# Performance work log

Measured on AMD Instinct MI355X. Metric: run time of the kernel, lower is better.

Reference implementation:

```python
import jax, jax.numpy as jnp
import numpy as np

CH = 16

_SOBEL_X = jnp.array([[-1.0, 0.0, 1.0], [-2.0, 0.0, 2.0], [-1.0, 0.0, 1.0]], dtype=jnp.float32) / 8.0
_SOBEL_Y = _SOBEL_X.T


def _depthwise3x3(x, k2d):
    # x: (B, C, H, W); k2d: (3, 3). Depthwise cross-correlation, padding=1 (matches torch.conv2d).
    c = x.shape[1]
    w = jnp.broadcast_to(k2d[None, None], (c, 1, 3, 3))
    return jax.lax.conv_general_dilated(
        x, w, window_strides=(1, 1), padding=((1, 1), (1, 1)),
        dimension_numbers=("NCHW", "OIHW", "NCHW"), feature_group_count=c)


def setup_inputs() -> dict:
    key = jax.random.key(0)
    k0, k1, k2, k3, k4 = jax.random.split(key, 5)
    B, C, H, W = 16, CH, 256, 256
    grid = jax.random.normal(k0, (B, C, H, W), dtype=jnp.float32)
    # 1x1 convs are per-pixel matmuls; store as matrices. Kaiming-ish scale.
    W1 = jax.random.normal(k1, (8 * CH, 3 * CH), dtype=jnp.float32) * (1.0 / np.sqrt(3 * CH))
    b1 = jax.random.normal(k2, (8 * CH,), dtype=jnp.float32) * 0.01
    W2 = jax.random.normal(k3, (CH, 8 * CH), dtype=jnp.float32) * (1.0 / np.sqrt(8 * CH))
    b2 = jax.random.normal(k4, (CH,), dtype=jnp.float32) * 0.01
    return {"grid": grid, "W1": W1, "b1": b1, "W2": W2, "b2": b2}


def reference(grid, W1, b1, W2, b2):
    # perception: concat(grid, sobel_x(grid), sobel_y(grid)) along channels -> (B, 3C, H, W)
    px = _depthwise3x3(grid, _SOBEL_X)
    py = _depthwise3x3(grid, _SOBEL_Y)
    perception = jnp.concatenate([grid, px, py], axis=1)
    # two-layer 1x1-conv MLP with ReLU
    h = jnp.einsum("bchw,oc->bohw", perception, W1) + b1[None, :, None, None]
    h = jax.nn.relu(h)
    out = jnp.einsum("bchw,oc->bohw", h, W2) + b2[None, :, None, None]
    return out
```

## Files before the change

### kernel.cpp

```cpp
#include <hip/hip_runtime.h>

typedef float           f32x16  __attribute__((ext_vector_type(16)));
typedef float           f32x4   __attribute__((ext_vector_type(4)));
typedef __bf16          bf16x8  __attribute__((ext_vector_type(8)));
typedef unsigned short  ushort8 __attribute__((ext_vector_type(8)));
typedef unsigned int    uint4v  __attribute__((ext_vector_type(4)));

#define MFMA(a,b,c) __builtin_amdgcn_mfma_f32_32x32x16_bf16(a, b, c, 0, 0, 0)

__device__ __forceinline__ unsigned fbits(float x) { return __builtin_bit_cast(unsigned, x); }
__device__ __forceinline__ float bitsf(unsigned u) { return __builtin_bit_cast(float, u); }

__device__ __forceinline__ void bsplit(float x, unsigned short& hi, unsigned short& lo) {
    unsigned u = fbits(x);
    hi = (unsigned short)(u >> 16);
    float rem = x - bitsf(u & 0xFFFF0000u);
    lo = (unsigned short)(fbits(rem) >> 16);
}

__global__ __launch_bounds__(256, 4) void nca_mfma3_kernel(
    const float* __restrict__ grid,
    const float* __restrict__ W1, const float* __restrict__ b1,
    const float* __restrict__ W2, const float* __restrict__ b2,
    float* __restrict__ out)
{
    __shared__ unsigned short sLDS[16640];
    float* sB1f = (float*)&sLDS[16384];

    const int tid  = threadIdx.x;
    const int l    = tid & 63;
    const int w    = tid >> 6;
    const int half = l >> 5;
    const int ol   = l & 31;

    #pragma unroll
    for (int i = 0; i < 3; ++i) {
        int sidx = tid + 256*i;
        int ls   = sidx & 63;
        int fp   = sidx >> 6;
        int kk   = fp % 3;
        int o    = (fp/3)*32 + (ls & 31);
        int k0   = kk*16 + (ls>>5)*8;
        float sc = (kk == 0) ? 1.0f : 0.125f;
        ushort8 hi8, lo8;
        #pragma unroll
        for (int j = 0; j < 8; ++j) {
            float v = W1[o*48 + k0 + j] * sc;
            unsigned short h, lo_;
            bsplit(v, h, lo_);
            hi8[j] = h; lo8[j] = lo_;
        }
        *(ushort8*)&sLDS[(fp*2 + 0)*512 + ls*8] = hi8;
        *(ushort8*)&sLDS[(fp*2 + 1)*512 + ls*8] = lo8;
    }

    {
        int kk2  = tid >> 5;
        int cidx = tid & 31;
        int o    = cidx & 15;
        int hs   = cidx >> 4;
        int k0   = kk2*16 + hs*8;
        ushort8 hi8, lo8;
        #pragma unroll
        for (int j = 0; j < 8; ++j) {
            float v = W2[o*128 + k0 + j];
            unsigned short h, lo_;
            bsplit(v, h, lo_);
            hi8[j] = h; lo8[j] = lo_;
        }
        *(ushort8*)&sLDS[12288 + (kk2*2 + 0)*256 + cidx*8] = hi8;
        *(ushort8*)&sLDS[12288 + (kk2*2 + 1)*256 + cidx*8] = lo8;
    }

    if (tid < 128) sB1f[tid] = b1[tid];

    const bool  v16 = (ol < 16);
    const float b2v = v16 ? b2[ol] : 0.0f;

    __syncthreads();

    const int w1a = l*16;
    const int w2a = 24576 + ((ol & 15) + (half << 4))*16;
    const int b1a = 4*half;

    const auto ld8 = [&](int byteoff) -> ushort8 {
        return *(const ushort8*)((const char*)sLDS + byteoff);
    };

    const int bid  = blockIdx.x;
    const int wgid = ((bid & 7) << 8) | (bid >> 3);

    const int gw = wgid*4 + w;
    const int t0 = gw*4;
    const int y  = (t0 >> 3) & 255;
    const int b  =  t0 >> 11;
    const int dyt = (y > 0)   ? -256 : 0;
    const int dyb = (y < 255) ?  256 : 0;
    const float fmt = (y > 0)   ? 1.f : 0.f;
    const float fmb = (y < 255) ? 1.f : 0.f;

    for (int i = 0; i < 4; ++i) {
        const int t  = t0 + i;
        const int x0 = (t & 7) << 5;
        const int x  = x0 + ol;

        const int   dxl = (x > 0)   ? -1 : 0;
        const int   dxr = (x < 255) ?  1 : 0;
        const float fml = (x > 0)   ? 1.f : 0.f;
        const float fmr = (x < 255) ? 1.f : 0.f;
        const float ftl = fml*fmt, ftr = fmr*fmt, fbl = fml*fmb, fbr = fmr*fmb;

        int w1ai = w1a, w2ai = w2a, b1ai = b1a;
        asm volatile("" : "+v"(w1ai), "+v"(w2ai), "+v"(b1ai));

        const int pbase = (b*16 + half*8)*65536 + y*256 + x;
        ushort8 ahi[3], alo[3];
        #pragma unroll
        for (int ci = 0; ci < 8; ++ci) {
            int ic = pbase + ci*65536;
            int it = ic + dyt, ib = ic + dyb;
            float v00 = grid[it + dxl]*ftl, v01 = grid[it]*fmt, v02 = grid[it + dxr]*ftr;
            float v10 = grid[ic + dxl]*fml, v11 = grid[ic],     v12 = grid[ic + dxr]*fmr;
            float v20 = grid[ib + dxl]*fbl, v21 = grid[ib]*fmb, v22 = grid[ib + dxr]*fbr;
            float sx = (v02 - v00) + 2.f*(v12 - v10) + (v22 - v20);
            float sy = (v20 - v00) + 2.f*(v21 - v01) + (v22 - v02);
            unsigned short h, lo_;
            bsplit(v11, h, lo_); ahi[0][ci] = h; alo[0][ci] = lo_;
            bsplit(sx,  h, lo_); ahi[1][ci] = h; alo[1][ci] = lo_;
            bsplit(sy,  h, lo_); ahi[2][ci] = h; alo[2][ci] = lo_;
        }

        f32x16 acc2;
        #pragma unroll
        for (int r = 0; r < 16; ++r) acc2[r] = b2v;

        #pragma unroll
        for (int og = 0; og < 4; ++og) {
            f32x16 acc1;
            #pragma unroll
            for (int T = 0; T < 4; ++T) {
                f32x4 q = *(const f32x4*)&sB1f[b1ai + og*32 + 8*T];
                acc1[4*T+0] = q[0]; acc1[4*T+1] = q[1];
                acc1[4*T+2] = q[2]; acc1[4*T+3] = q[3];
            }

            #pragma unroll
            for (int kk = 0; kk < 3; ++kk) {
                bf16x8 ph  = __builtin_bit_cast(bf16x8, ahi[kk]);
                bf16x8 pl  = __builtin_bit_cast(bf16x8, alo[kk]);
                bf16x8 w_h = __builtin_bit_cast(bf16x8, ld8(w1ai + ((og*3 + kk)*2 + 0)*1024));
                bf16x8 w_l = __builtin_bit_cast(bf16x8, ld8(w1ai + ((og*3 + kk)*2 + 1)*1024));
                acc1 = MFMA(w_h, ph, acc1);
                acc1 = MFMA(w_h, pl, acc1);
                acc1 = MFMA(w_l, ph, acc1);
            }

            unsigned Phi[8], Plo[8];
            #pragma unroll
            for (int T = 0; T < 4; ++T) {
                float h0 = fmaxf(acc1[4*T+0], 0.f), h1 = fmaxf(acc1[4*T+1], 0.f);
                float h2 = fmaxf(acc1[4*T+2], 0.f), h3 = fmaxf(acc1[4*T+3], 0.f);
                unsigned u0 = fbits(h0), u1 = fbits(h1), u2 = fbits(h2), u3 = fbits(h3);
                Phi[2*T+0] = (u0 >> 16) | (u1 & 0xFFFF0000u);
                Phi[2*T+1] = (u2 >> 16) | (u3 & 0xFFFF0000u);
                float r0 = h0 - bitsf(u0 & 0xFFFF0000u);
                float r1 = h1 - bitsf(u1 & 0xFFFF0000u);
                float r2 = h2 - bitsf(u2 & 0xFFFF0000u);
                float r3 = h3 - bitsf(u3 & 0xFFFF0000u);
                Plo[2*T+0] = (fbits(r0) >> 16) | (fbits(r1) & 0xFFFF0000u);
                Plo[2*T+1] = (fbits(r2) >> 16) | (fbits(r3) & 0xFFFF0000u);
            }

            #pragma unroll
            for (int c = 0; c < 2; ++c) {
                unsigned fa0 = Phi[(2*c)*2+0], fb0 = Phi[(2*c+1)*2+0];
                unsigned fa1 = Phi[(2*c)*2+1], fb1 = Phi[(2*c+1)*2+1];
                asm volatile("v_permlane32_swap_b32 %0, %1" : "+v"(fa0), "+v"(fb0));
                asm volatile("v_permlane32_swap_b32 %0, %1" : "+v"(fa1), "+v"(fb1));
                unsigned la0 = Plo[(2*c)*2+0], lb0 = Plo[(2*c+1)*2+0];
                unsigned la1 = Plo[(2*c)*2+1], lb1 = Plo[(2*c+1)*2+1];
                asm volatile("v_permlane32_swap_b32 %0, %1" : "+v"(la0), "+v"(lb0));
                asm volatile("v_permlane32_swap_b32 %0, %1" : "+v"(la1), "+v"(lb1));
                uint4v hv_ = { fa0, fa1, fb0, fb1 };
                uint4v lv_ = { la0, la1, lb0, lb1 };
                bf16x8 A2h = __builtin_bit_cast(bf16x8, hv_);
                bf16x8 A2l = __builtin_bit_cast(bf16x8, lv_);

                const int g = (og*2 + c)*2;
                bf16x8 w2h = __builtin_bit_cast(bf16x8, ld8(w2ai + (g + 0)*512));
                bf16x8 w2l = __builtin_bit_cast(bf16x8, ld8(w2ai + (g + 1)*512));
                acc2 = MFMA(A2h, w2h, acc2);
                acc2 = MFMA(A2h, w2l, acc2);
                acc2 = MFMA(A2l, w2h, acc2);
            }
        }

        if (v16) {
            const int ob = (b*16 + ol)*65536 + y*256 + x0 + half*4;
            #pragma unroll
            for (int c = 0; c < 4; ++c) {
                f32x4 v = { acc2[4*c+0], acc2[4*c+1], acc2[4*c+2], acc2[4*c+3] };
                *(f32x4*)&out[ob + c*8] = v;
            }
        }
    }
}

extern "C" void kernel_launch(void* const* d_in, const int* in_sizes, int n_in,
                              void* d_out, int out_size, void* d_ws, size_t ws_size,
                              hipStream_t stream) {
    const float* grid = (const float*)d_in[0];
    const float* W1   = (const float*)d_in[1];
    const float* b1   = (const float*)d_in[2];
    const float* W2   = (const float*)d_in[3];
    const float* b2   = (const float*)d_in[4];
    float* out = (float*)d_out;

    nca_mfma3_kernel<<<2048, 256, 0, stream>>>(grid, W1, b1, W2, b2, out);
}
```

Measured before the change: 191.4 us.

## Use 512-thread blocks, add branch-free interior stencil path, and pack bf16 halves with v_perm

```diff
diff --git a/kernel.cpp b/kernel.cpp
--- a/kernel.cpp
+++ b/kernel.cpp
@@ -8,17 +8,24 @@
 
 #define MFMA(a,b,c) __builtin_amdgcn_mfma_f32_32x32x16_bf16(a, b, c, 0, 0, 0)
 
-__device__ __forceinline__ unsigned fbits(float x) { return __builtin_bit_cast(unsigned, x); }
-__device__ __forceinline__ float bitsf(unsigned u) { return __builtin_bit_cast(float, u); }
-
-__device__ __forceinline__ void bsplit(float x, unsigned short& hi, unsigned short& lo) {
+static __device__ __forceinline__ unsigned fbits(float x) { return __builtin_bit_cast(unsigned, x); }
+static __device__ __forceinline__ float    bitsf(unsigned u) { return __builtin_bit_cast(float, u); }
+
+static __device__ __forceinline__ void bsplit(float x, unsigned short& hi, unsigned short& lo) {
     unsigned u = fbits(x);
     hi = (unsigned short)(u >> 16);
     float rem = x - bitsf(u & 0xFFFF0000u);
     lo = (unsigned short)(fbits(rem) >> 16);
 }
 
-__global__ __launch_bounds__(256, 4) void nca_mfma3_kernel(
+static __device__ __forceinline__ unsigned packhi(float e, float o) {
+    return __builtin_amdgcn_perm(fbits(o), fbits(e), 0x07060302u);
+}
+static __device__ __forceinline__ float remf(float x) {
+    return x - bitsf(fbits(x) & 0xFFFF0000u);
+}
+
+__global__ __launch_bounds__(512, 8) void nca_mfma4_kernel(
     const float* __restrict__ grid,
     const float* __restrict__ W1, const float* __restrict__ b1,
     const float* __restrict__ W2, const float* __restrict__ b2,
@@ -33,9 +40,7 @@
     const int half = l >> 5;
     const int ol   = l & 31;
 
-    #pragma unroll
-    for (int i = 0; i < 3; ++i) {
-        int sidx = tid + 256*i;
+    for (int sidx = tid; sidx < 768; sidx += 512) {
         int ls   = sidx & 63;
         int fp   = sidx >> 6;
         int kk   = fp % 3;
@@ -45,16 +50,15 @@
         ushort8 hi8, lo8;
         #pragma unroll
         for (int j = 0; j < 8; ++j) {
-            float v = W1[o*48 + k0 + j] * sc;
             unsigned short h, lo_;
-            bsplit(v, h, lo_);
+            bsplit(W1[o*48 + k0 + j] * sc, h, lo_);
             hi8[j] = h; lo8[j] = lo_;
         }
         *(ushort8*)&sLDS[(fp*2 + 0)*512 + ls*8] = hi8;
         *(ushort8*)&sLDS[(fp*2 + 1)*512 + ls*8] = lo8;
     }
 
-    {
+    if (tid < 256) {
         int kk2  = tid >> 5;
         int cidx = tid & 31;
         int o    = cidx & 15;
@@ -63,9 +67,8 @@
         ushort8 hi8, lo8;
         #pragma unroll
         for (int j = 0; j < 8; ++j) {
-            float v = W2[o*128 + k0 + j];
             unsigned short h, lo_;
-            bsplit(v, h, lo_);
+            bsplit(W2[o*128 + k0 + j], h, lo_);
             hi8[j] = h; lo8[j] = lo_;
         }
         *(ushort8*)&sLDS[12288 + (kk2*2 + 0)*256 + cidx*8] = hi8;
@@ -88,9 +91,9 @@
     };
 
     const int bid  = blockIdx.x;
-    const int wgid = ((bid & 7) << 8) | (bid >> 3);
-
-    const int gw = wgid*4 + w;
+    const int wgid = ((bid & 7) << 7) | (bid >> 3);
+
+    const int gw = wgid*8 + w;
     const int t0 = gw*4;
     const int y  = (t0 >> 3) & 255;
     const int b  =  t0 >> 11;
@@ -104,30 +107,69 @@
         const int x0 = (t & 7) << 5;
         const int x  = x0 + ol;
 
-        const int   dxl = (x > 0)   ? -1 : 0;
-        const int   dxr = (x < 255) ?  1 : 0;
-        const float fml = (x > 0)   ? 1.f : 0.f;
-        const float fmr = (x < 255) ? 1.f : 0.f;
-        const float ftl = fml*fmt, ftr = fmr*fmt, fbl = fml*fmb, fbr = fmr*fmb;
-
         int w1ai = w1a, w2ai = w2a, b1ai = b1a;
         asm volatile("" : "+v"(w1ai), "+v"(w2ai), "+v"(b1ai));
 
-        const int pbase = (b*16 + half*8)*65536 + y*256 + x;
-        ushort8 ahi[3], alo[3];
-        #pragma unroll
-        for (int ci = 0; ci < 8; ++ci) {
-            int ic = pbase + ci*65536;
-            int it = ic + dyt, ib = ic + dyb;
-            float v00 = grid[it + dxl]*ftl, v01 = grid[it]*fmt, v02 = grid[it + dxr]*ftr;
-            float v10 = grid[ic + dxl]*fml, v11 = grid[ic],     v12 = grid[ic + dxr]*fmr;
-            float v20 = grid[ib + dxl]*fbl, v21 = grid[ib]*fmb, v22 = grid[ib + dxr]*fbr;
-            float sx = (v02 - v00) + 2.f*(v12 - v10) + (v22 - v20);
-            float sy = (v20 - v00) + 2.f*(v21 - v01) + (v22 - v02);
-            unsigned short h, lo_;
-            bsplit(v11, h, lo_); ahi[0][ci] = h; alo[0][ci] = lo_;
-            bsplit(sx,  h, lo_); ahi[1][ci] = h; alo[1][ci] = lo_;
-            bsplit(sy,  h, lo_); ahi[2][ci] = h; alo[2][ci] = lo_;
+        bf16x8 pah[3], pal[3];
+
+        const bool interior = (x0 != 0) && (x0 != 224) && (y != 0) && (y != 255);
+        if (interior) {
+            const float* p = grid + ((b*16 + half*8)*65536 + y*256 + x);
+            unsigned A[3][4], L[3][4];
+            #pragma unroll
+            for (int cp = 0; cp < 4; ++cp) {
+                const float* pe = p;
+                const float* po = p + 65536;
+                float e00 = pe[-257], e01 = pe[-256], e02 = pe[-255];
+                float e10 = pe[-1],   e11 = pe[0],    e12 = pe[1];
+                float e20 = pe[255],  e21 = pe[256],  e22 = pe[257];
+                float o00 = po[-257], o01 = po[-256], o02 = po[-255];
+                float o10 = po[-1],   o11 = po[0],    o12 = po[1];
+                float o20 = po[255],  o21 = po[256],  o22 = po[257];
+                float esx = (e02 - e00) + 2.f*(e12 - e10) + (e22 - e20);
+                float esy = (e20 - e00) + 2.f*(e21 - e01) + (e22 - e02);
+                float osx = (o02 - o00) + 2.f*(o12 - o10) + (o22 - o20);
+                float osy = (o20 - o00) + 2.f*(o21 - o01) + (o22 - o02);
+                A[0][cp] = packhi(e11, o11); L[0][cp] = packhi(remf(e11), remf(o11));
+                A[1][cp] = packhi(esx, osx); L[1][cp] = packhi(remf(esx), remf(osx));
+                A[2][cp] = packhi(esy, osy); L[2][cp] = packhi(remf(esy), remf(osy));
+                p += 2*65536;
+            }
+            #pragma unroll
+            for (int kk = 0; kk < 3; ++kk) {
+                uint4v ha = { A[kk][0], A[kk][1], A[kk][2], A[kk][3] };
+                uint4v la = { L[kk][0], L[kk][1], L[kk][2], L[kk][3] };
+                pah[kk] = __builtin_bit_cast(bf16x8, ha);
+                pal[kk] = __builtin_bit_cast(bf16x8, la);
+            }
+        } else {
+            const int   dxl = (x > 0)   ? -1 : 0;
+            const int   dxr = (x < 255) ?  1 : 0;
+            const float fml = (x > 0)   ? 1.f : 0.f;
+            const float fmr = (x < 255) ? 1.f : 0.f;
+            const float ftl = fml*fmt, ftr = fmr*fmt, fbl = fml*fmb, fbr = fmr*fmb;
+
+            const int pbase = (b*16 + half*8)*65536 + y*256 + x;
+            ushort8 ahi[3], alo[3];
+            #pragma unroll
+            for (int ci = 0; ci < 8; ++ci) {
+                int ic = pbase + ci*65536;
+                int it = ic + dyt, ib = ic + dyb;
+                float v00 = grid[it + dxl]*ftl, v01 = grid[it]*fmt, v02 = grid[it + dxr]*ftr;
+                float v10 = grid[ic + dxl]*fml, v11 = grid[ic],     v12 = grid[ic + dxr]*fmr;
+                float v20 = grid[ib + dxl]*fbl, v21 = grid[ib]*fmb, v22 = grid[ib + dxr]*fbr;
+                float sx = (v02 - v00) + 2.f*(v12 - v10) + (v22 - v20);
+                float sy = (v20 - v00) + 2.f*(v21 - v01) + (v22 - v02);
+                unsigned short h, lo_;
+                bsplit(v11, h, lo_); ahi[0][ci] = h; alo[0][ci] = lo_;
+                bsplit(sx,  h, lo_); ahi[1][ci] = h; alo[1][ci] = lo_;
+                bsplit(sy,  h, lo_); ahi[2][ci] = h; alo[2][ci] = lo_;
+            }
+            #pragma unroll
+            for (int kk = 0; kk < 3; ++kk) {
+                pah[kk] = __builtin_bit_cast(bf16x8, ahi[kk]);
+                pal[kk] = __builtin_bit_cast(bf16x8, alo[kk]);
+            }
         }
 
         f32x16 acc2;
@@ -146,13 +188,11 @@
 
             #pragma unroll
             for (int kk = 0; kk < 3; ++kk) {
-                bf16x8 ph  = __builtin_bit_cast(bf16x8, ahi[kk]);
-                bf16x8 pl  = __builtin_bit_cast(bf16x8, alo[kk]);
                 bf16x8 w_h = __builtin_bit_cast(bf16x8, ld8(w1ai + ((og*3 + kk)*2 + 0)*1024));
                 bf16x8 w_l = __builtin_bit_cast(bf16x8, ld8(w1ai + ((og*3 + kk)*2 + 1)*1024));
-                acc1 = MFMA(w_h, ph, acc1);
-                acc1 = MFMA(w_h, pl, acc1);
-                acc1 = MFMA(w_l, ph, acc1);
+                acc1 = MFMA(w_h, pah[kk], acc1);
+                acc1 = MFMA(w_h, pal[kk], acc1);
+                acc1 = MFMA(w_l, pah[kk], acc1);
             }
 
             unsigned Phi[8], Plo[8];
@@ -160,15 +200,10 @@
             for (int T = 0; T < 4; ++T) {
                 float h0 = fmaxf(acc1[4*T+0], 0.f), h1 = fmaxf(acc1[4*T+1], 0.f);
                 float h2 = fmaxf(acc1[4*T+2], 0.f), h3 = fmaxf(acc1[4*T+3], 0.f);
-                unsigned u0 = fbits(h0), u1 = fbits(h1), u2 = fbits(h2), u3 = fbits(h3);
-                Phi[2*T+0] = (u0 >> 16) | (u1 & 0xFFFF0000u);
-                Phi[2*T+1] = (u2 >> 16) | (u3 & 0xFFFF0000u);
-                float r0 = h0 - bitsf(u0 & 0xFFFF0000u);
-                float r1 = h1 - bitsf(u1 & 0xFFFF0000u);
-                float r2 = h2 - bitsf(u2 & 0xFFFF0000u);
-                float r3 = h3 - bitsf(u3 & 0xFFFF0000u);
-                Plo[2*T+0] = (fbits(r0) >> 16) | (fbits(r1) & 0xFFFF0000u);
-                Plo[2*T+1] = (fbits(r2) >> 16) | (fbits(r3) & 0xFFFF0000u);
+                Phi[2*T+0] = packhi(h0, h1);
+                Phi[2*T+1] = packhi(h2, h3);
+                Plo[2*T+0] = packhi(remf(h0), remf(h1));
+                Plo[2*T+1] = packhi(remf(h2), remf(h3));
             }
 
             #pragma unroll
@@ -216,5 +251,5 @@
     const float* b2   = (const float*)d_in[4];
     float* out = (float*)d_out;
 
-    nca_mfma3_kernel<<<2048, 256, 0, stream>>>(grid, W1, b1, W2, b2, out);
-}
+    nca_mfma4_kernel<<<1024, 512, 0, stream>>>(grid, W1, b1, W2, b2, out);
+}
```

Measured after the change: 394.9 us. 2.06x slower.
